# Kernel optimization log

Hardware: AMD Instinct MI355X
Metric: run time of the kernel (lower is better)

Reference implementation:

```python
import jax, jax.numpy as jnp
import numpy as np
import math

B, SQ, SK, D, H = 2, 2048, 2048, 1024, 16
DH = D // H
EPS = 1e-5

def _ln(x, g, b):
    m = jnp.mean(x, axis=-1, keepdims=True)
    v = jnp.mean(jnp.square(x - m), axis=-1, keepdims=True)
    return (x - m) / jnp.sqrt(v + EPS) * g + b

def setup_inputs() -> dict:
    key = jax.random.key(0)
    ks = jax.random.split(key, 8)
    xav = math.sqrt(6.0 / (D + D))  # xavier_uniform for square [D,D] weights
    inp = {
        'Q': jax.random.normal(ks[0], (B, SQ, D), dtype=jnp.float32),
        'K': jax.random.normal(ks[1], (B, SK, D), dtype=jnp.float32),
        'pad_mask': jax.random.randint(ks[2], (B, SK), 0, 2, dtype=jnp.int32),
        'Wq': jax.random.uniform(ks[3], (D, D), jnp.float32, -xav, xav),
        'Wk': jax.random.uniform(ks[4], (D, D), jnp.float32, -xav, xav),
        'Wv': jax.random.uniform(ks[5], (D, D), jnp.float32, -xav, xav),
        'Wo': jax.random.uniform(ks[6], (D, D), jnp.float32, -xav, xav),
        'bq': jnp.zeros((D,), jnp.float32),
        'bk': jnp.zeros((D,), jnp.float32),
        'bv': jnp.zeros((D,), jnp.float32),
        'bo': jnp.zeros((D,), jnp.float32),
        'ln_q_g': jnp.ones((D,), jnp.float32),  'ln_q_b': jnp.zeros((D,), jnp.float32),
        'ln_kv_g': jnp.ones((D,), jnp.float32), 'ln_kv_b': jnp.zeros((D,), jnp.float32),
        'ln_f_g': jnp.ones((D,), jnp.float32),  'ln_f_b': jnp.zeros((D,), jnp.float32),
    }
    return inp

def reference(Q, K, pad_mask, Wq, Wk, Wv, Wo, bq, bk, bv, bo,
              ln_q_g, ln_q_b, ln_kv_g, ln_kv_b, ln_f_g, ln_f_b):
    Q_ = _ln(Q, ln_q_g, ln_q_b)
    K_ = _ln(K, ln_kv_g, ln_kv_b)
    # projections (PyTorch Linear: x @ W.T + b)
    Q1 = (Q_ @ Wq.T + bq).reshape(B, SQ, H, DH)
    K1 = (K_ @ Wk.T + bk).reshape(B, SK, H, DH)
    V1 = (K_ @ Wv.T + bv).reshape(B, SK, H, DH)
    # note: scaling uses sqrt(dim_V), NOT sqrt(head_dim), per source
    score = jnp.einsum('bqhd,bkhd->bhqk', Q1, K1) / math.sqrt(D)
    m = pad_mask[:, None, None, :]  # [B,1,1,SK]
    score = jnp.where(m == 0, jnp.float32(-1e12), score)
    A = jax.nn.softmax(score, axis=-1)
    A = A * m.astype(A.dtype)  # second mask application after softmax
    O1 = jnp.einsum('bhqk,bkhd->bqhd', A, V1).reshape(B, SQ, D)
    O2 = jax.nn.relu(Q_ @ Wo.T + bo)
    return _ln(Q + O1 + O2, ln_f_g, ln_f_b)
```

## Files before the change

### kernel.cpp

```cpp
#include <hip/hip_runtime.h>
#include <stdint.h>

#define NB 2
#define NSQ 2048
#define NSK 2048
#define ND 1024
#define NH 16
#define NDH 64

typedef unsigned short u16;
typedef unsigned int u32;
typedef __bf16 bf16x8_t __attribute__((ext_vector_type(8)));
typedef float f32x4_t __attribute__((ext_vector_type(4)));
typedef u32 u32x4_t __attribute__((ext_vector_type(4)));

#define AS1 __attribute__((address_space(1)))
#define AS3 __attribute__((address_space(3)))

__device__ __forceinline__ float bf2f(u16 u) {
    union { float f; u32 i; } v; v.i = ((u32)u) << 16; return v.f;
}
__device__ __forceinline__ u16 f2bf(float x) {
    union { float f; u32 i; } v; v.f = x;
    u32 r = v.i + 0x7fffu + ((v.i >> 16) & 1u);
    return (u16)(r >> 16);
}
__device__ __forceinline__ u32 fbits(float x) {
    union { float f; u32 i; } v; v.f = x; return v.i;
}

__global__ __launch_bounds__(256) void detect_kernel(
    const u16* __restrict__ Q, int* __restrict__ flag)
{
    __shared__ int s;
    if (threadIdx.x == 0) s = 0;
    __syncthreads();
    uint2 x = ((const uint2*)Q)[threadIdx.x];
    u16 a0 = x.x & 0xffff, a1 = x.x >> 16, a2 = x.y & 0xffff, a3 = x.y >> 16;
    bool big = (((a0 >> 7) & 0xff) >= 0x8D) || (((a1 >> 7) & 0xff) >= 0x8D) ||
               (((a2 >> 7) & 0xff) >= 0x8D) || (((a3 >> 7) & 0xff) >= 0x8D);
    if (big) s = 1;
    __syncthreads();
    if (threadIdx.x == 0) *flag = s;
}

__global__ __launch_bounds__(256) void cvt_params_kernel(
    const int* __restrict__ flag,
    const void* __restrict__ Wq, const void* __restrict__ Wk,
    const void* __restrict__ Wv, const void* __restrict__ Wo,
    const void* __restrict__ vbq, const void* __restrict__ vbk,
    const void* __restrict__ vbv, const void* __restrict__ vbo,
    const void* __restrict__ g0, const void* __restrict__ b0,
    const void* __restrict__ g1, const void* __restrict__ b1,
    const void* __restrict__ g2, const void* __restrict__ b2,
    u16* __restrict__ Wc, u16* __restrict__ Vc)
{
    int blk = blockIdx.x;
    int t = threadIdx.x;
    const void* src;
    u16* dst;
    size_t srcoff;
    if (blk < 4096) {
        int w = blk >> 10;
        src = (w == 0) ? Wq : (w == 1) ? Wk : (w == 2) ? Wv : Wo;
        srcoff = (size_t)(blk & 1023) * 1024;
        dst = Wc + (size_t)w * 1024 * 1024 + srcoff;
    } else {
        int v = blk - 4096;
        src = (v == 0) ? vbq : (v == 1) ? vbk : (v == 2) ? vbv : (v == 3) ? vbo :
              (v == 4) ? g0  : (v == 5) ? b0  : (v == 6) ? g1  : (v == 7) ? b1 :
              (v == 8) ? g2  : b2;
        srcoff = 0;
        dst = Vc + (size_t)v * 1024;
    }
    u32 lo, hi;
    if (*flag) {
        float4 x = ((const float4*)src)[srcoff / 4 + t];
        lo = (u32)f2bf(x.x) | ((u32)f2bf(x.y) << 16);
        hi = (u32)f2bf(x.z) | ((u32)f2bf(x.w) << 16);
    } else {
        uint2 x = ((const uint2*)src)[srcoff / 4 + t];
        lo = x.x; hi = x.y;
    }
    uint2 o; o.x = lo; o.y = hi;
    ((uint2*)dst)[t] = o;
}

__global__ __launch_bounds__(256) void idx_kernel(
    const int* __restrict__ mask, int* __restrict__ idx, int* __restrict__ cnt)
{
    int b = blockIdx.x;
    const int* m = mask + b * NSK;
    int t = threadIdx.x;
    int loc[8]; int s = 0;
#pragma unroll
    for (int i = 0; i < 8; ++i) { loc[i] = (m[t * 8 + i] != 0); s += loc[i]; }
    __shared__ int ps[256];
    ps[t] = s;
    __syncthreads();
    for (int off = 1; off < 256; off <<= 1) {
        int v = (t >= off) ? ps[t - off] : 0;
        __syncthreads();
        ps[t] += v;
        __syncthreads();
    }
    int run = ps[t] - s;
#pragma unroll
    for (int i = 0; i < 8; ++i)
        if (loc[i]) idx[b * NSK + run++] = t * 8 + i;
    if (t == 255) cnt[b] = ps[255];
}

__global__ __launch_bounds__(256) void ln_in_kernel(
    const int* __restrict__ flag,
    const void* __restrict__ Q, const void* __restrict__ K,
    const u16* __restrict__ Vc,
    u16* __restrict__ Qn, u16* __restrict__ Kn)
{
    int row = blockIdx.x;
    const void* x; const u16 *g, *bb; u16* y;
    size_t roff;
    if (row < NB * NSQ) {
        x = Q; roff = (size_t)row * ND;
        g = Vc + 4 * 1024; bb = Vc + 5 * 1024;
        y = Qn + roff;
    } else {
        int r2 = row - NB * NSQ;
        x = K; roff = (size_t)r2 * ND;
        g = Vc + 6 * 1024; bb = Vc + 7 * 1024;
        y = Kn + roff;
    }
    int t = threadIdx.x;
    float v0, v1, v2, v3;
    if (*flag) {
        float4 xv = ((const float4*)x)[roff / 4 + t];
        v0 = xv.x; v1 = xv.y; v2 = xv.z; v3 = xv.w;
    } else {
        uint2 ux = ((const uint2*)x)[roff / 4 + t];
        v0 = bf2f(ux.x & 0xffff); v1 = bf2f(ux.x >> 16);
        v2 = bf2f(ux.y & 0xffff); v3 = bf2f(ux.y >> 16);
    }
    float s1 = v0 + v1 + v2 + v3;
    float s2 = v0*v0 + v1*v1 + v2*v2 + v3*v3;
#pragma unroll
    for (int off = 32; off >= 1; off >>= 1) {
        s1 += __shfl_xor(s1, off);
        s2 += __shfl_xor(s2, off);
    }
    __shared__ float r1[4], r2[4];
    int wave = t >> 6;
    if ((t & 63) == 0) { r1[wave] = s1; r2[wave] = s2; }
    __syncthreads();
    float t1 = r1[0] + r1[1] + r1[2] + r1[3];
    float t2 = r2[0] + r2[1] + r2[2] + r2[3];
    float mean = t1 * (1.0f / ND);
    float var  = t2 * (1.0f / ND) - mean * mean;
    float rstd = rsqrtf(var + 1e-5f);
    uint2 ug = ((const uint2*)g)[t];
    uint2 ub = ((const uint2*)bb)[t];
    float y0 = (v0 - mean) * rstd * bf2f(ug.x & 0xffff) + bf2f(ub.x & 0xffff);
    float y1 = (v1 - mean) * rstd * bf2f(ug.x >> 16)    + bf2f(ub.x >> 16);
    float y2 = (v2 - mean) * rstd * bf2f(ug.y & 0xffff) + bf2f(ub.y & 0xffff);
    float y3 = (v3 - mean) * rstd * bf2f(ug.y >> 16)    + bf2f(ub.y >> 16);
    uint2 o;
    o.x = (u32)f2bf(y0) | ((u32)f2bf(y1) << 16);
    o.y = (u32)f2bf(y2) | ((u32)f2bf(y3) << 16);
    ((uint2*)y)[t] = o;
}

__global__ __launch_bounds__(512, 2) void gemm4_kernel(
    const u16* __restrict__ Qn, const u16* __restrict__ Kn,
    const u16* __restrict__ Wc, const u16* __restrict__ Vc,
    u16* __restrict__ Q1, u16* __restrict__ K1, u16* __restrict__ V1,
    u16* __restrict__ R)
{
    int z = blockIdx.z;
    const u16* X    = (z == 0 || z == 3) ? Qn : Kn;
    const u16* W    = Wc + (size_t)z * 1024 * 1024;
    const u16* bias = Vc + (size_t)z * 1024;

    __shared__ u16 sm[4][2][256 * 32];

    int tid  = threadIdx.x;
    int wave = tid >> 6, lane = tid & 63;
    int wm = wave >> 2, wn = wave & 3;
    int quad = lane >> 4, l4 = lane & 15;
    int m0 = blockIdx.x * 256;
    int n0 = blockIdx.y * 256;

    int srow   = wave * 16 + (lane >> 2);
    int schunk = (lane & 3) ^ ((srow >> 1) & 3);
    const u16* gA = X + (size_t)(m0 + srow) * ND + schunk * 8;
    const u16* gB = W + (size_t)(n0 + srow) * ND + schunk * 8;

#define STAGE_A(t_) do { int s_ = (t_) & 3; \
    __builtin_amdgcn_global_load_lds((const AS1 u32*)(gA + (t_) * 32), \
        (AS3 u32*)(&sm[s_][0][wave * 512]), 16, 0, 0); \
    __builtin_amdgcn_global_load_lds((const AS1 u32*)(gA + (t_) * 32 + (size_t)128 * ND), \
        (AS3 u32*)(&sm[s_][0][4096 + wave * 512]), 16, 0, 0); \
} while (0)
#define STAGE_B(t_) do { int s_ = (t_) & 3; \
    __builtin_amdgcn_global_load_lds((const AS1 u32*)(gB + (t_) * 32), \
        (AS3 u32*)(&sm[s_][1][wave * 512]), 16, 0, 0); \
    __builtin_amdgcn_global_load_lds((const AS1 u32*)(gB + (t_) * 32 + (size_t)128 * ND), \
        (AS3 u32*)(&sm[s_][1][4096 + wave * 512]), 16, 0, 0); \
} while (0)

    int fch   = (quad ^ ((l4 >> 1) & 3)) * 8;
    int aoffb = (wm * 128 + l4) * 32 + fch;
    int boffb = (wn * 64  + l4) * 32 + fch;

    f32x4_t acc[8][4];
#pragma unroll
    for (int i = 0; i < 8; ++i)
#pragma unroll
        for (int j = 0; j < 4; ++j)
            acc[i][j] = (f32x4_t){0.f, 0.f, 0.f, 0.f};

    STAGE_A(0); STAGE_B(0);
    STAGE_A(1); STAGE_B(1);
    STAGE_A(2); STAGE_B(2);
    asm volatile("s_waitcnt vmcnt(8)" ::: "memory");
    __builtin_amdgcn_s_barrier();
    __builtin_amdgcn_sched_barrier(0);

    for (int t = 0; t < 32; ++t) {
        const u16* a = &sm[t & 3][0][0];
        const u16* b = &sm[t & 3][1][0];
        bf16x8_t bf[4], af[4];

#pragma unroll
        for (int nf = 0; nf < 4; ++nf)
            bf[nf] = *(const bf16x8_t*)(b + boffb + nf * 512);
#pragma unroll
        for (int mf = 0; mf < 4; ++mf)
            af[mf] = *(const bf16x8_t*)(a + aoffb + mf * 512);
        if (t < 29) STAGE_A(t + 3);
        __builtin_amdgcn_s_barrier();
        __builtin_amdgcn_s_setprio(1);
#pragma unroll
        for (int mf = 0; mf < 4; ++mf)
#pragma unroll
            for (int nf = 0; nf < 4; ++nf)
                acc[mf][nf] = __builtin_amdgcn_mfma_f32_16x16x32_bf16(
                    af[mf], bf[nf], acc[mf][nf], 0, 0, 0);
        __builtin_amdgcn_s_setprio(0);
        __builtin_amdgcn_s_barrier();

#pragma unroll
        for (int mf = 0; mf < 4; ++mf)
            af[mf] = *(const bf16x8_t*)(a + aoffb + (mf + 4) * 512);
        if (t < 29) STAGE_B(t + 3);
        __builtin_amdgcn_s_barrier();
        __builtin_amdgcn_s_setprio(1);
#pragma unroll
        for (int mf = 0; mf < 4; ++mf)
#pragma unroll
            for (int nf = 0; nf < 4; ++nf)
                acc[mf + 4][nf] = __builtin_amdgcn_mfma_f32_16x16x32_bf16(
                    af[mf], bf[nf], acc[mf + 4][nf], 0, 0, 0);
        __builtin_amdgcn_s_setprio(0);

        if (t < 29)       asm volatile("s_waitcnt vmcnt(8)" ::: "memory");
        else if (t == 29) asm volatile("s_waitcnt vmcnt(4)" ::: "memory");
        else if (t == 30) asm volatile("s_waitcnt vmcnt(0)" ::: "memory");
        __builtin_amdgcn_s_barrier();
        __builtin_amdgcn_sched_barrier(0);
    }
#undef STAGE_A
#undef STAGE_B

    u16* outp = (z == 0) ? Q1 : (z == 1) ? K1 : (z == 2) ? V1 : R;
#pragma unroll
    for (int nf = 0; nf < 4; ++nf) {
        int n = n0 + wn * 64 + nf * 16 + l4;
        float bv_ = bf2f(bias[n]);
#pragma unroll
        for (int mf = 0; mf < 8; ++mf) {
#pragma unroll
            for (int r = 0; r < 4; ++r) {
                int m = m0 + wm * 128 + mf * 16 + quad * 4 + r;
                float val = acc[mf][nf][r] + bv_;
                if (z == 0) val *= 0.045105964f;
                if (z == 3) val = fmaxf(val, 0.f);
                outp[(size_t)m * ND + n] = f2bf(val);
            }
        }
    }
}

__global__ __launch_bounds__(256) void gather_k_kernel(
    const u16* __restrict__ K1, const int* __restrict__ idx,
    const int* __restrict__ cnt, u16* __restrict__ Kc)
{
    int b = blockIdx.y;
    int c = cnt[b];
    int cPad = (c + 63) & ~63;
    int jb = blockIdx.x * 16;
    if (jb >= cPad) return;
    int t = threadIdx.x;
    int row = t >> 4;
    int seg = t & 15;
    int j = jb + row;
    if (j >= cPad) return;
    bool z = (j >= c);
    const u16* src = z ? (const u16*)0
        : K1 + ((size_t)b * NSK + idx[(size_t)b * NSK + j]) * ND;
    u16* dst = Kc + ((size_t)b * NSK + j) * ND;
#pragma unroll
    for (int i = 0; i < 8; ++i) {
        int off = (seg * 8 + i) * 8;
        uint4 v = z ? (uint4){0, 0, 0, 0} : *(const uint4*)(src + off);
        *(uint4*)(dst + off) = v;
    }
}

__global__ __launch_bounds__(256) void gather_vt_kernel(
    const u16* __restrict__ V1, const int* __restrict__ idx,
    const int* __restrict__ cnt, u16* __restrict__ Vct)
{
    int kb = blockIdx.x;
    int h  = blockIdx.y;
    int b  = blockIdx.z;
    int c = cnt[b];
    int cPad = (c + 63) & ~63;
    if (kb * 64 >= cPad) return;
    __shared__ u16 sT[64 * 72];
    int tid = threadIdx.x;
    {
        int row = tid >> 3, seg = tid & 7;
        int j1 = kb * 64 + row, j2 = j1 + 32;
        uint4 v1 = {0, 0, 0, 0}, v2 = {0, 0, 0, 0};
        if (j1 < c) v1 = *(const uint4*)(V1 +
            ((size_t)b * NSK + idx[(size_t)b * NSK + j1]) * ND + h * NDH + seg * 8);
        if (j2 < c) v2 = *(const uint4*)(V1 +
            ((size_t)b * NSK + idx[(size_t)b * NSK + j2]) * ND + h * NDH + seg * 8);
        *(uint4*)(sT + row * 72 + seg * 8) = v1;
        *(uint4*)(sT + (row + 32) * 72 + seg * 8) = v2;
    }
    __syncthreads();
    int d = tid >> 2, sg = tid & 3;
    u16 buf[16];
#pragma unroll
    for (int i = 0; i < 8; ++i) buf[i]     = sT[(sg * 8 + i) * 72 + d];
#pragma unroll
    for (int i = 0; i < 8; ++i) buf[8 + i] = sT[((sg + 4) * 8 + i) * 72 + d];
    u16* go = Vct + ((size_t)(b * NH + h) * NDH + d) * NSK + kb * 64;
    *(uint4*)(go + sg * 8)       = *(uint4*)buf;
    *(uint4*)(go + (sg + 4) * 8) = *(uint4*)(buf + 8);
}

__global__ __launch_bounds__(256, 4) void attn_kernel(
    const u16* __restrict__ Q1, const u16* __restrict__ Kc,
    const u16* __restrict__ Vct, const int* __restrict__ cnt,
    u16* __restrict__ R)
{
    int q0 = blockIdx.x * 64;
    int h  = blockIdx.y;
    int b  = blockIdx.z;

    __shared__ u16 sK[2][64 * 64];
    __shared__ u16 sV[2][64 * 64];

    int tid  = threadIdx.x;
    int wave = tid >> 6, lane = tid & 63;
    int quad = lane >> 4, l4 = lane & 15;
    int lk = lane >> 3, ls = lane & 7;
    int gseg = ls ^ lk;

    int c  = cnt[b];
    int nt = (c + 63) >> 6;

    bf16x8_t qf[2];
    {
        const u16* qp = Q1 + (size_t)(b * NSQ + q0 + wave * 16 + l4) * ND + h * NDH;
        qf[0] = *(const bf16x8_t*)(qp + quad * 8);
        qf[1] = *(const bf16x8_t*)(qp + 32 + quad * 8);
    }

    const u16* kbase = Kc + (size_t)b * NSK * ND + h * NDH;
    const u16* vbase = Vct + (size_t)(b * NH + h) * NDH * NSK;

    const u16* gk0 = kbase + (size_t)(wave * 16 + lk) * ND + gseg * 8;
    const u16* gk1 = gk0 + (size_t)8 * ND;
    const u16* gv0 = vbase + (size_t)(wave * 16 + lk) * NSK + gseg * 8;
    const u16* gv1 = gv0 + (size_t)8 * NSK;

    int fragOff[2];
#pragma unroll
    for (int kk = 0; kk < 2; ++kk)
        fragOff[kk] = l4 * 64 + (((kk * 4 + quad) ^ (l4 & 7)) * 8);

    float l_run = 0.f;
    f32x4_t acc_o[4];
#pragma unroll
    for (int T = 0; T < 4; ++T) acc_o[T] = (f32x4_t){0.f, 0.f, 0.f, 0.f};

    int srcA = (quad & 1) * 32 + l4;
    int srcB = srcA + 16;
    bool hi = lane >= 32;

    if (nt > 0) {
        __builtin_amdgcn_global_load_lds((const AS1 u32*)gk0,
            (AS3 u32*)(&sK[0][(wave * 16) * 64]), 16, 0, 0);
        __builtin_amdgcn_global_load_lds((const AS1 u32*)gk1,
            (AS3 u32*)(&sK[0][(wave * 16 + 8) * 64]), 16, 0, 0);
        __builtin_amdgcn_global_load_lds((const AS1 u32*)gv0,
            (AS3 u32*)(&sV[0][(wave * 16) * 64]), 16, 0, 0);
        __builtin_amdgcn_global_load_lds((const AS1 u32*)gv1,
            (AS3 u32*)(&sV[0][(wave * 16 + 8) * 64]), 16, 0, 0);
        gk0 += (size_t)64 * ND; gk1 += (size_t)64 * ND;
        gv0 += 64; gv1 += 64;

        for (int kb = 0; kb < nt; ++kb) {
            __syncthreads();

            if (kb + 1 < nt) {
                int bi = (kb + 1) & 1;
                __builtin_amdgcn_global_load_lds((const AS1 u32*)gk0,
                    (AS3 u32*)(&sK[bi][(wave * 16) * 64]), 16, 0, 0);
                __builtin_amdgcn_global_load_lds((const AS1 u32*)gk1,
                    (AS3 u32*)(&sK[bi][(wave * 16 + 8) * 64]), 16, 0, 0);
                __builtin_amdgcn_global_load_lds((const AS1 u32*)gv0,
                    (AS3 u32*)(&sV[bi][(wave * 16) * 64]), 16, 0, 0);
                __builtin_amdgcn_global_load_lds((const AS1 u32*)gv1,
                    (AS3 u32*)(&sV[bi][(wave * 16 + 8) * 64]), 16, 0, 0);
                gk0 += (size_t)64 * ND; gk1 += (size_t)64 * ND;
                gv0 += 64; gv1 += 64;
            }

            const u16* kt = sK[kb & 1];
            const u16* vt = sV[kb & 1];

            f32x4_t accs[4];
            if (kb == nt - 1) {
#pragma unroll
                for (int tm = 0; tm < 4; ++tm) {
                    int key = kb * 64 + tm * 16 + quad * 4;
#pragma unroll
                    for (int r = 0; r < 4; ++r)
                        accs[tm][r] = (key + r < c) ? 0.f : -1e9f;
                }
            } else {
#pragma unroll
                for (int tm = 0; tm < 4; ++tm)
                    accs[tm] = (f32x4_t){0.f, 0.f, 0.f, 0.f};
            }
#pragma unroll
            for (int kk = 0; kk < 2; ++kk)
#pragma unroll
                for (int tm = 0; tm < 4; ++tm) {
                    bf16x8_t kf = *(const bf16x8_t*)(kt + tm * 1024 + fragOff[kk]);
                    accs[tm] = __builtin_amdgcn_mfma_f32_16x16x32_bf16(
                        kf, qf[kk], accs[tm], 0, 0, 0);
                }

            float lsum = 0.f;
            u32 pk[4][2];
#pragma unroll
            for (int tm = 0; tm < 4; ++tm) {
                float p0 = exp2f(accs[tm][0]);
                float p1 = exp2f(accs[tm][1]);
                float p2 = exp2f(accs[tm][2]);
                float p3 = exp2f(accs[tm][3]);
                lsum += p0 + p1 + p2 + p3;
                pk[tm][0] = __builtin_amdgcn_perm(fbits(p1), fbits(p0), 0x07060302);
                pk[tm][1] = __builtin_amdgcn_perm(fbits(p3), fbits(p2), 0x07060302);
            }
            lsum += __shfl_xor(lsum, 16);
            lsum += __shfl_xor(lsum, 32);
            l_run += lsum;

#pragma unroll
            for (int kk = 0; kk < 2; ++kk) {
                u32 a0 = __shfl((int)pk[kk * 2][0], srcA), a1 = __shfl((int)pk[kk * 2][1], srcA);
                u32 b0 = __shfl((int)pk[kk * 2 + 1][0], srcA), b1 = __shfl((int)pk[kk * 2 + 1][1], srcA);
                u32 c0 = __shfl((int)pk[kk * 2][0], srcB), c1 = __shfl((int)pk[kk * 2][1], srcB);
                u32 d0 = __shfl((int)pk[kk * 2 + 1][0], srcB), d1 = __shfl((int)pk[kk * 2 + 1][1], srcB);
                u32x4_t pr;
                pr.x = hi ? b0 : a0;
                pr.y = hi ? b1 : a1;
                pr.z = hi ? d0 : c0;
                pr.w = hi ? d1 : c1;
                bf16x8_t pf = __builtin_bit_cast(bf16x8_t, pr);
#pragma unroll
                for (int T = 0; T < 4; ++T) {
                    bf16x8_t vf = *(const bf16x8_t*)(vt + T * 1024 + fragOff[kk]);
                    acc_o[T] = __builtin_amdgcn_mfma_f32_16x16x32_bf16(
                        vf, pf, acc_o[T], 0, 0, 0);
                }
            }
        }
    }

    float inv = l_run > 0.f ? 1.f / l_run : 0.f;
    u16* rp = R + (size_t)(b * NSQ + q0 + wave * 16 + l4) * ND + h * NDH;
#pragma unroll
    for (int T = 0; T < 4; ++T) {
        u16* p = rp + T * 16 + quad * 4;
        uint2 o2 = *(const uint2*)p;
        float e0 = acc_o[T][0] * inv + bf2f(o2.x & 0xffff);
        float e1 = acc_o[T][1] * inv + bf2f(o2.x >> 16);
        float e2 = acc_o[T][2] * inv + bf2f(o2.y & 0xffff);
        float e3 = acc_o[T][3] * inv + bf2f(o2.y >> 16);
        uint2 on;
        on.x = (u32)f2bf(e0) | ((u32)f2bf(e1) << 16);
        on.y = (u32)f2bf(e2) | ((u32)f2bf(e3) << 16);
        *(uint2*)p = on;
    }
}

__global__ __launch_bounds__(256) void ln_out_kernel(
    const int* __restrict__ flag,
    const void* __restrict__ Q, const u16* __restrict__ R,
    const u16* __restrict__ Vc, void* __restrict__ out)
{
    int row = blockIdx.x;
    size_t roff = (size_t)row * ND;
    int t = threadIdx.x;
    int f = *flag;
    float v0, v1, v2, v3;
    uint2 ur = ((const uint2*)(R + roff))[t];
    if (f) {
        float4 xq = ((const float4*)Q)[roff / 4 + t];
        v0 = xq.x; v1 = xq.y; v2 = xq.z; v3 = xq.w;
    } else {
        uint2 uq = ((const uint2*)Q)[roff / 4 + t];
        v0 = bf2f(uq.x & 0xffff); v1 = bf2f(uq.x >> 16);
        v2 = bf2f(uq.y & 0xffff); v3 = bf2f(uq.y >> 16);
    }
    v0 += bf2f(ur.x & 0xffff); v1 += bf2f(ur.x >> 16);
    v2 += bf2f(ur.y & 0xffff); v3 += bf2f(ur.y >> 16);
    float s1 = v0 + v1 + v2 + v3;
    float s2 = v0*v0 + v1*v1 + v2*v2 + v3*v3;
#pragma unroll
    for (int off = 32; off >= 1; off >>= 1) {
        s1 += __shfl_xor(s1, off);
        s2 += __shfl_xor(s2, off);
    }
    __shared__ float r1[4], r2[4];
    int wave = t >> 6;
    if ((t & 63) == 0) { r1[wave] = s1; r2[wave] = s2; }
    __syncthreads();
    float t1 = r1[0] + r1[1] + r1[2] + r1[3];
    float t2 = r2[0] + r2[1] + r2[2] + r2[3];
    float mean = t1 * (1.0f / ND);
    float var  = t2 * (1.0f / ND) - mean * mean;
    float rstd = rsqrtf(var + 1e-5f);
    const u16* g  = Vc + 8 * 1024;
    const u16* bb = Vc + 9 * 1024;
    uint2 ug = ((const uint2*)g)[t];
    uint2 ub = ((const uint2*)bb)[t];
    float y0 = (v0 - mean) * rstd * bf2f(ug.x & 0xffff) + bf2f(ub.x & 0xffff);
    float y1 = (v1 - mean) * rstd * bf2f(ug.x >> 16)    + bf2f(ub.x >> 16);
    float y2 = (v2 - mean) * rstd * bf2f(ug.y & 0xffff) + bf2f(ub.y & 0xffff);
    float y3 = (v3 - mean) * rstd * bf2f(ug.y >> 16)    + bf2f(ub.y >> 16);
    if (f) {
        float4 o; o.x = y0; o.y = y1; o.z = y2; o.w = y3;
        ((float4*)out)[roff / 4 + t] = o;
    } else {
        uint2 o;
        o.x = (u32)f2bf(y0) | ((u32)f2bf(y1) << 16);
        o.y = (u32)f2bf(y2) | ((u32)f2bf(y3) << 16);
        ((uint2*)out)[roff / 4 + t] = o;
    }
}

extern "C" void kernel_launch(void* const* d_in, const int* in_sizes, int n_in,
                              void* d_out, int out_size, void* d_ws, size_t ws_size,
                              hipStream_t stream) {
    const void* Q        = d_in[0];
    const void* K        = d_in[1];
    const int* pad_mask  = (const int*)d_in[2];

    const size_t NEL = (size_t)NB * NSQ * ND;
    int* flag = (int*)d_ws;
    int* cnt  = flag + 1;
    int* idx  = flag + 4;
    u16* base = (u16*)(idx + 4096);
    u16* Qn  = base;
    u16* Kn  = Qn + NEL;
    u16* Q1  = Kn + NEL;
    u16* K1  = Q1 + NEL;
    u16* V1  = K1 + NEL;
    u16* R   = V1 + NEL;
    u16* Wc  = R + NEL;
    u16* Vc  = Wc + (size_t)4 * 1024 * 1024;
    u16* Kc  = Qn;
    u16* Vct = Kn;

    detect_kernel<<<dim3(1), dim3(256), 0, stream>>>((const u16*)Q, flag);

    cvt_params_kernel<<<dim3(4106), dim3(256), 0, stream>>>(
        flag, d_in[3], d_in[4], d_in[5], d_in[6],
        d_in[7], d_in[8], d_in[9], d_in[10],
        d_in[11], d_in[12], d_in[13], d_in[14], d_in[15], d_in[16],
        Wc, Vc);

    idx_kernel<<<dim3(NB), dim3(256), 0, stream>>>(pad_mask, idx, cnt);

    ln_in_kernel<<<dim3(2 * NB * NSQ), dim3(256), 0, stream>>>(
        flag, Q, K, Vc, Qn, Kn);

    gemm4_kernel<<<dim3(16, 4, 4), dim3(512), 0, stream>>>(
        Qn, Kn, Wc, Vc, Q1, K1, V1, R);

    gather_k_kernel<<<dim3(128, NB), dim3(256), 0, stream>>>(K1, idx, cnt, Kc);

    gather_vt_kernel<<<dim3(32, NH, NB), dim3(256), 0, stream>>>(V1, idx, cnt, Vct);

    attn_kernel<<<dim3(NSQ / 64, NH, NB), dim3(256), 0, stream>>>(
        Q1, Kc, Vct, cnt, R);

    ln_out_kernel<<<dim3(NB * NSQ), dim3(256), 0, stream>>>(
        flag, Q, R, Vc, d_out);
}
```

Before: 240.7 us.

## Remap GEMM block order for L2 locality and merge per-step barriers

Block indices are remapped so that consecutive workgroups are spread across XCD-like groups of 8 (u = (lin&7)*32 + lin>>3), changing which tiles of the four projections run concurrently and which share cache. The inner k-loop now loads all A fragments at once and issues both A and B LDS stages together, dropping two of the three barriers per iteration to reduce synchronisation stalls. The price is four extra vector registers for the second half of A. The epilogue is reordered so bias values are loaded once and stores are grouped by row.

New measurement: 231.4 us. 3.8% less time.

```diff
diff --git a/kernel.cpp b/kernel.cpp
--- a/kernel.cpp
+++ b/kernel.cpp
@@ -174,7 +174,12 @@
     u16* __restrict__ Q1, u16* __restrict__ K1, u16* __restrict__ V1,
     u16* __restrict__ R)
 {
-    int z = blockIdx.z;
+    int lin = blockIdx.x + 16 * blockIdx.y + 64 * blockIdx.z;
+    int u   = (lin & 7) * 32 + (lin >> 3);
+    int bx  = u & 15;
+    int by  = (u >> 4) & 3;
+    int z   = u >> 6;
+
     const u16* X    = (z == 0 || z == 3) ? Qn : Kn;
     const u16* W    = Wc + (size_t)z * 1024 * 1024;
     const u16* bias = Vc + (size_t)z * 1024;
@@ -185,8 +190,8 @@
     int wave = tid >> 6, lane = tid & 63;
     int wm = wave >> 2, wn = wave & 3;
     int quad = lane >> 4, l4 = lane & 15;
-    int m0 = blockIdx.x * 256;
-    int n0 = blockIdx.y * 256;
+    int m0 = bx * 256;
+    int n0 = by * 256;
 
     int srow   = wave * 16 + (lane >> 2);
     int schunk = (lane & 3) ^ ((srow >> 1) & 3);
@@ -227,7 +232,7 @@
     for (int t = 0; t < 32; ++t) {
         const u16* a = &sm[t & 3][0][0];
         const u16* b = &sm[t & 3][1][0];
-        bf16x8_t bf[4], af[4];
+        bf16x8_t bf[4], af[4], ah[4];
 
 #pragma unroll
         for (int nf = 0; nf < 4; ++nf)
@@ -235,8 +240,12 @@
 #pragma unroll
         for (int mf = 0; mf < 4; ++mf)
             af[mf] = *(const bf16x8_t*)(a + aoffb + mf * 512);
-        if (t < 29) STAGE_A(t + 3);
-        __builtin_amdgcn_s_barrier();
+#pragma unroll
+        for (int mf = 0; mf < 4; ++mf)
+            ah[mf] = *(const bf16x8_t*)(a + aoffb + (mf + 4) * 512);
+
+        if (t < 29) { STAGE_A(t + 3); STAGE_B(t + 3); }
+
         __builtin_amdgcn_s_setprio(1);
 #pragma unroll
         for (int mf = 0; mf < 4; ++mf)
@@ -244,21 +253,12 @@
             for (int nf = 0; nf < 4; ++nf)
                 acc[mf][nf] = __builtin_amdgcn_mfma_f32_16x16x32_bf16(
                     af[mf], bf[nf], acc[mf][nf], 0, 0, 0);
-        __builtin_amdgcn_s_setprio(0);
-        __builtin_amdgcn_s_barrier();
-
-#pragma unroll
-        for (int mf = 0; mf < 4; ++mf)
-            af[mf] = *(const bf16x8_t*)(a + aoffb + (mf + 4) * 512);
-        if (t < 29) STAGE_B(t + 3);
-        __builtin_amdgcn_s_barrier();
-        __builtin_amdgcn_s_setprio(1);
 #pragma unroll
         for (int mf = 0; mf < 4; ++mf)
 #pragma unroll
             for (int nf = 0; nf < 4; ++nf)
                 acc[mf + 4][nf] = __builtin_amdgcn_mfma_f32_16x16x32_bf16(
-                    af[mf], bf[nf], acc[mf + 4][nf], 0, 0, 0);
+                    ah[mf], bf[nf], acc[mf + 4][nf], 0, 0, 0);
         __builtin_amdgcn_s_setprio(0);
 
         if (t < 29)       asm volatile("s_waitcnt vmcnt(8)" ::: "memory");
@@ -271,16 +271,19 @@
 #undef STAGE_B
 
     u16* outp = (z == 0) ? Q1 : (z == 1) ? K1 : (z == 2) ? V1 : R;
-#pragma unroll
-    for (int nf = 0; nf < 4; ++nf) {
-        int n = n0 + wn * 64 + nf * 16 + l4;
-        float bv_ = bf2f(bias[n]);
-#pragma unroll
-        for (int mf = 0; mf < 8; ++mf) {
-#pragma unroll
-            for (int r = 0; r < 4; ++r) {
-                int m = m0 + wm * 128 + mf * 16 + quad * 4 + r;
-                float val = acc[mf][nf][r] + bv_;
+    float bv_[4];
+#pragma unroll
+    for (int nf = 0; nf < 4; ++nf)
+        bv_[nf] = bf2f(bias[n0 + wn * 64 + nf * 16 + l4]);
+#pragma unroll
+    for (int mf = 0; mf < 8; ++mf) {
+#pragma unroll
+        for (int r = 0; r < 4; ++r) {
+            int m = m0 + wm * 128 + mf * 16 + quad * 4 + r;
+#pragma unroll
+            for (int nf = 0; nf < 4; ++nf) {
+                int n = n0 + wn * 64 + nf * 16 + l4;
+                float val = acc[mf][nf][r] + bv_[nf];
                 if (z == 0) val *= 0.045105964f;
                 if (z == 3) val = fmaxf(val, 0.f);
                 outp[(size_t)m * ND + n] = f2bf(val);
```
